# Kernel tuning notes

Measured on AMD Instinct MI355X. Metric: run time of the kernel, lower is better.

The kernel has to match this reference:

```python
import jax, jax.numpy as jnp
import numpy as np
from jax import lax

T, B, D, H = 1024, 64, 512, 512


def _elman_layer(x_seq, Wih, bih, Whh, bhh):
    """x_seq: [T, B, in]; returns hidden sequence [T, B, out].
    Input-side GEMM is precomputed across all timesteps; the recurrence
    (h @ Whh^T + bhh, tanh) runs in a lax.scan with state resident.
    """
    xs = jnp.einsum('tbi,hi->tbh', x_seq, Wih) + bih  # [T, B, H]
    h0 = jnp.zeros((x_seq.shape[1], Whh.shape[0]), dtype=x_seq.dtype)

    def step(h, xt):
        h_new = jnp.tanh(xt + h @ Whh.T + bhh)
        return h_new, h_new

    _, ys = lax.scan(step, h0, xs)
    return ys


def setup_inputs() -> dict:
    key = jax.random.key(0)
    ks = jax.random.split(key, 9)
    stdv = 1.0 / np.sqrt(H)
    u = lambda k, shape: jax.random.uniform(k, shape, jnp.float32, -stdv, stdv)
    return {
        'Xt': jax.random.normal(ks[0], (T, B, D), jnp.float32),
        'ihW0': u(ks[1], (H, D)),
        'ihB0': u(ks[2], (H,)),
        'hhW0': u(ks[3], (H, H)),
        'hhB0': u(ks[4], (H,)),
        'ihW1': u(ks[5], (H, H)),
        'ihB1': u(ks[6], (H,)),
        'hhW1': u(ks[7], (H, H)),
        'hhB1': u(ks[8], (H,)),
    }


def reference(Xt, ihW0, ihB0, hhW0, hhB0, ihW1, ihB1, hhW1, hhB1):
    # 2-layer Elman RNN, tanh activation, zero initial hidden state,
    # dropout=0 (eval), stack_output=True -> output [T, B, H].
    y0 = _elman_layer(Xt, ihW0, ihB0, hhW0, hhB0)
    y1 = _elman_layer(y0, ihW1, ihB1, hhW1, hhB1)
    return y1
```

## Files before the change

kernel.cpp:

```cpp
#include <hip/hip_runtime.h>
#include <math.h>
#include <stdint.h>

#define TT      1024
#define BATCH   64
#define HH      512
#define NG      8
#define WPG     32
#define BSL     8
#define HSL     16
#define NTH     512

#define WBLK(m, jj, u)  ((((m) * 2 + (jj)) * 4 + (u)) << 10)
#define WLDS    (24 * 1024)
#define SPW     516
#define BUFH0   WLDS
#define BUFH1   (WLDS + 8 * SPW)
#define SCR     (WLDS + 16 * SPW)
#define SCRS    17
#define LDS_FL  (SCR + 129 * SCRS)
#define LDS_BYTES (LDS_FL * 4)

__device__ __forceinline__ float2 sys_ld2(const float* p) {
    unsigned long long v = __hip_atomic_load((const unsigned long long*)p, __ATOMIC_RELAXED,
                                             __HIP_MEMORY_SCOPE_SYSTEM);
    union { unsigned long long u; float2 f; } cv; cv.u = v; return cv.f;
}
__device__ __forceinline__ void sys_st(float* p, float v) {
    __hip_atomic_store(p, v, __ATOMIC_RELAXED, __HIP_MEMORY_SCOPE_SYSTEM);
}
__device__ __forceinline__ void wait_vm0() {
    asm volatile("s_waitcnt vmcnt(0)" ::: "memory");
}
__device__ __forceinline__ void dot4(float4 w, float4 x, float& a) {
    a = fmaf(w.x, x.x, a); a = fmaf(w.y, x.y, a);
    a = fmaf(w.z, x.z, a); a = fmaf(w.w, x.w, a);
}

__global__ void __launch_bounds__(256)
z0_gemm(const float* __restrict__ X, const float* __restrict__ W,
        const float* __restrict__ bih, float* __restrict__ Z)
{
    __shared__ float As[32][68];
    __shared__ float Bs[32][68];
    const int tid = threadIdx.x;
    const int tx  = tid & 15, ty = tid >> 4;
    const int n0  = (blockIdx.x & 7) * 64;
    const int m0  = (blockIdx.x >> 3) * 64;
    const int lm  = tid >> 3;
    const int lk  = (tid & 7) * 4;

    float4 bb;
    bb.x = bih[n0 + tx * 4 + 0]; bb.y = bih[n0 + tx * 4 + 1];
    bb.z = bih[n0 + tx * 4 + 2]; bb.w = bih[n0 + tx * 4 + 3];

    float acc[4][4];
    #pragma unroll
    for (int i = 0; i < 4; ++i)
        #pragma unroll
        for (int j = 0; j < 4; ++j) acc[i][j] = 0.f;

    for (int k0 = 0; k0 < 512; k0 += 32) {
        float4 a0 = *(const float4*)(X + (size_t)(m0 + lm) * 512 + k0 + lk);
        float4 a1 = *(const float4*)(X + (size_t)(m0 + lm + 32) * 512 + k0 + lk);
        float4 b0 = *(const float4*)(W + (size_t)(n0 + lm) * 512 + k0 + lk);
        float4 b1 = *(const float4*)(W + (size_t)(n0 + lm + 32) * 512 + k0 + lk);
        __syncthreads();
        As[lk + 0][lm] = a0.x; As[lk + 1][lm] = a0.y;
        As[lk + 2][lm] = a0.z; As[lk + 3][lm] = a0.w;
        As[lk + 0][lm + 32] = a1.x; As[lk + 1][lm + 32] = a1.y;
        As[lk + 2][lm + 32] = a1.z; As[lk + 3][lm + 32] = a1.w;
        Bs[lk + 0][lm] = b0.x; Bs[lk + 1][lm] = b0.y;
        Bs[lk + 2][lm] = b0.z; Bs[lk + 3][lm] = b0.w;
        Bs[lk + 0][lm + 32] = b1.x; Bs[lk + 1][lm + 32] = b1.y;
        Bs[lk + 2][lm + 32] = b1.z; Bs[lk + 3][lm + 32] = b1.w;
        __syncthreads();
        #pragma unroll
        for (int kk = 0; kk < 32; ++kk) {
            float4 av = *(const float4*)(&As[kk][ty * 4]);
            float4 bv = *(const float4*)(&Bs[kk][tx * 4]);
            acc[0][0] = fmaf(av.x, bv.x, acc[0][0]); acc[0][1] = fmaf(av.x, bv.y, acc[0][1]);
            acc[0][2] = fmaf(av.x, bv.z, acc[0][2]); acc[0][3] = fmaf(av.x, bv.w, acc[0][3]);
            acc[1][0] = fmaf(av.y, bv.x, acc[1][0]); acc[1][1] = fmaf(av.y, bv.y, acc[1][1]);
            acc[1][2] = fmaf(av.y, bv.z, acc[1][2]); acc[1][3] = fmaf(av.y, bv.w, acc[1][3]);
            acc[2][0] = fmaf(av.z, bv.x, acc[2][0]); acc[2][1] = fmaf(av.z, bv.y, acc[2][1]);
            acc[2][2] = fmaf(av.z, bv.z, acc[2][2]); acc[2][3] = fmaf(av.z, bv.w, acc[2][3]);
            acc[3][0] = fmaf(av.w, bv.x, acc[3][0]); acc[3][1] = fmaf(av.w, bv.y, acc[3][1]);
            acc[3][2] = fmaf(av.w, bv.z, acc[3][2]); acc[3][3] = fmaf(av.w, bv.w, acc[3][3]);
        }
    }
    #pragma unroll
    for (int i = 0; i < 4; ++i) {
        float4 r;
        r.x = acc[i][0] + bb.x; r.y = acc[i][1] + bb.y;
        r.z = acc[i][2] + bb.z; r.w = acc[i][3] + bb.w;
        *(float4*)(Z + (size_t)(m0 + ty * 4 + i) * 512 + n0 + tx * 4) = r;
    }
}

__global__ void __launch_bounds__(NTH, 2)
elman_persistent(const float* __restrict__ Whh0, const float* __restrict__ bhh0,
                 const float* __restrict__ Wih1, const float* __restrict__ bih1,
                 const float* __restrict__ Whh1, const float* __restrict__ bhh1,
                 float* __restrict__ out,
                 float* h0buf,
                 unsigned* cnt)
{
    extern __shared__ float lds[];
    const int tid = threadIdx.x;
    const int g   = blockIdx.x & 7;
    const int w   = blockIdx.x >> 3;
    const int jg0 = w * HSL;
    const int bg0 = g * BSL;

    const int jp   = tid & 7;
    const int bb4  = ((tid >> 3) & 1) * 4;
    const int ks   = tid >> 4;
    const int kb   = ks * 4;
    const int wofs = ks * 32 + jp * 4;
    const int lane = tid & 63;
    const int wv   = tid >> 6;

    const int row = tid >> 6;
    const int kst = (tid & 63) * 4;

    {
        const float* const Ws[3] = {Whh0, Wih1, Whh1};
        for (int f = tid; f < 48 * 128; f += NTH) {
            const int jrow = f >> 7, k4 = f & 127;
            const int mat = jrow >> 4, r = jrow & 15;
            const int jp_ = r >> 1, jj_ = r & 1;
            const int u_ = k4 >> 5, ks_ = k4 & 31;
            float4 v = ((const float4*)(Ws[mat] + (size_t)(jg0 + r) * HH))[k4];
            *(float4*)(lds + WBLK(mat, jj_, u_) + ks_ * 32 + jp_ * 4) = v;
        }
    }
    float bias = 0.f;
    if (tid < 256) {
        const int l = tid >> 7, jx = jg0 + (tid & 15);
        bias = l ? (bih1[jx] + bhh1[jx]) : bhh0[jx];
    }
    __syncthreads();

    const float* h1load = out + (size_t)(bg0 + row) * HH + kst;

    unsigned* mycnt = cnt + g * 64;
    unsigned target = 0;
    bool     dead   = false;

    for (int p = 0; p <= TT; ++p) {
        const bool doL0  = (p < TT);
        const bool doL1  = (p >= 1);
        const bool hasH1 = (p >= 2);
        const int  cur   = p & 1;

        float2 h0a, h0b, h0c, h0d;
        {
            const float* hs = h0buf + (size_t)((p + 1) & 1) * (BATCH * HH)
                            + (size_t)(bg0 + row) * HH + kst;
            h0a = sys_ld2(hs);       h0b = sys_ld2(hs + 2);
            h0c = sys_ld2(hs + 256); h0d = sys_ld2(hs + 258);
        }
        float2 h1a = {0.f, 0.f}, h1b = h1a, h1c = h1a, h1d = h1a;
        if (hasH1) {
            h1a = sys_ld2(h1load);       h1b = sys_ld2(h1load + 2);
            h1c = sys_ld2(h1load + 256); h1d = sys_ld2(h1load + 258);
            h1load += BATCH * HH;
        }
        float z0v = 0.f;
        if (doL0 && tid < 128)
            z0v = out[((size_t)p * BATCH + bg0 + (tid >> 4)) * HH + jg0 + (tid & 15)];

        wait_vm0();
        *(float4*)(lds + BUFH0 + row * SPW + kst)       = make_float4(h0a.x, h0a.y, h0b.x, h0b.y);
        *(float4*)(lds + BUFH0 + row * SPW + kst + 256) = make_float4(h0c.x, h0c.y, h0d.x, h0d.y);
        if (hasH1) {
            *(float4*)(lds + BUFH1 + row * SPW + kst)       = make_float4(h1a.x, h1a.y, h1b.x, h1b.y);
            *(float4*)(lds + BUFH1 + row * SPW + kst + 256) = make_float4(h1c.x, h1c.y, h1d.x, h1d.y);
        }
        __syncthreads();

        float acc0[2][4], acc1[2][4];
        #pragma unroll
        for (int jj = 0; jj < 2; ++jj)
            #pragma unroll
            for (int bi = 0; bi < 4; ++bi) { acc0[jj][bi] = 0.f; acc1[jj][bi] = 0.f; }

        auto h0pass = [&](bool d0, bool d1) {
            #pragma unroll
            for (int u = 0; u < 4; ++u) {
                float4 wa0 = *(const float4*)(lds + WBLK(0, 0, u) + wofs);
                float4 wa1 = *(const float4*)(lds + WBLK(0, 1, u) + wofs);
                float4 wb0 = *(const float4*)(lds + WBLK(1, 0, u) + wofs);
                float4 wb1 = *(const float4*)(lds + WBLK(1, 1, u) + wofs);
                #pragma unroll
                for (int bi = 0; bi < 4; ++bi) {
                    float4 hv = *(const float4*)(lds + BUFH0 + (bb4 + bi) * SPW + kb + u * 128);
                    if (d0) { dot4(wa0, hv, acc0[0][bi]);
                              dot4(wa1, hv, acc0[1][bi]); }
                    if (d1) { dot4(wb0, hv, acc1[0][bi]);
                              dot4(wb1, hv, acc1[1][bi]); }
                }
            }
        };
        if (doL0 && doL1) h0pass(true, true);
        else if (doL0)    h0pass(true, false);
        else              h0pass(false, true);
        if (hasH1) {
            #pragma unroll
            for (int u = 0; u < 4; ++u) {
                float4 wc0 = *(const float4*)(lds + WBLK(2, 0, u) + wofs);
                float4 wc1 = *(const float4*)(lds + WBLK(2, 1, u) + wofs);
                #pragma unroll
                for (int bi = 0; bi < 4; ++bi) {
                    float4 hv = *(const float4*)(lds + BUFH1 + (bb4 + bi) * SPW + kb + u * 128);
                    dot4(wc0, hv, acc1[0][bi]);
                    dot4(wc1, hv, acc1[1][bi]);
                }
            }
        }

        #pragma unroll
        for (int jj = 0; jj < 2; ++jj)
            #pragma unroll
            for (int bi = 0; bi < 4; ++bi) {
                acc0[jj][bi] += __shfl_xor(acc0[jj][bi], 16);
                acc0[jj][bi] += __shfl_xor(acc0[jj][bi], 32);
                acc1[jj][bi] += __shfl_xor(acc1[jj][bi], 16);
                acc1[jj][bi] += __shfl_xor(acc1[jj][bi], 32);
            }
        if (lane < 16) {
            #pragma unroll
            for (int jj = 0; jj < 2; ++jj)
                #pragma unroll
                for (int bi = 0; bi < 4; ++bi) {
                    lds[SCR + (wv * 16 + jj * 4 + bi) * SCRS + lane]     = acc0[jj][bi];
                    lds[SCR + (wv * 16 + 8 + jj * 4 + bi) * SCRS + lane] = acc1[jj][bi];
                }
        }
        __syncthreads();

        if (tid < 256) {
            const int l    = tid >> 7;
            const int jloc = tid & 15;
            const int blo  = (tid >> 4) & 7;
            const int a    = l * 8 + (jloc & 1) * 4 + (blo & 3);
            const int ll   = (jloc >> 1) + 8 * (blo >> 2);
            float s = 0.f;
            #pragma unroll
            for (int wq = 0; wq < 8; ++wq)
                s += lds[SCR + (wq * 16 + a) * SCRS + ll];
            float val = tanhf(s + bias + z0v);
            if (l == 0) {
                if (doL0) sys_st(h0buf + (size_t)cur * (BATCH * HH)
                                 + (size_t)(bg0 + blo) * HH + jg0 + jloc, val);
            } else {
                if (doL1) sys_st(out + ((size_t)(p - 1) * BATCH + bg0 + blo) * HH + jg0 + jloc, val);
            }
        }
        wait_vm0();
        __syncthreads();

        if (tid == 0) {
            __hip_atomic_fetch_add(mycnt, 1u, __ATOMIC_RELAXED, __HIP_MEMORY_SCOPE_SYSTEM);
            target += WPG;
            if (!dead) {
                unsigned spins = 0;
                while (__hip_atomic_load(mycnt, __ATOMIC_RELAXED, __HIP_MEMORY_SCOPE_SYSTEM) < target) {
                    __builtin_amdgcn_s_sleep(2);
                    if (++spins > (1u << 21)) { dead = true; break; }
                }
            }
            asm volatile("" ::: "memory");
        } else {
            target += WPG;
        }
        __syncthreads();
    }
}

extern "C" void kernel_launch(void* const* d_in, const int* in_sizes, int n_in,
                              void* d_out, int out_size, void* d_ws, size_t ws_size,
                              hipStream_t stream) {
    (void)in_sizes; (void)n_in; (void)out_size; (void)ws_size;
    const float* Xt   = (const float*)d_in[0];
    const float* Wih0 = (const float*)d_in[1];
    const float* bih0 = (const float*)d_in[2];
    const float* Whh0 = (const float*)d_in[3];
    const float* bhh0 = (const float*)d_in[4];
    const float* Wih1 = (const float*)d_in[5];
    const float* bih1 = (const float*)d_in[6];
    const float* Whh1 = (const float*)d_in[7];
    const float* bhh1 = (const float*)d_in[8];
    float*    out   = (float*)d_out;
    float*    h0buf = (float*)d_ws;
    unsigned* cnt   = (unsigned*)((char*)d_ws + 2 * BATCH * HH * 4);

    hipFuncSetAttribute((const void*)elman_persistent,
                        hipFuncAttributeMaxDynamicSharedMemorySize, LDS_BYTES);
    hipMemsetAsync(d_ws, 0, 2 * BATCH * HH * 4 + NG * 256, stream);

    z0_gemm<<<dim3((TT * BATCH / 64) * (HH / 64)), dim3(256), 0, stream>>>(
        Xt, Wih0, bih0, out);

    elman_persistent<<<dim3(NG * WPG), dim3(NTH), LDS_BYTES, stream>>>(
        Whh0, bhh0, Wih1, bih1, Whh1, bhh1, out, h0buf, cnt);
}
```

Before: 6.995 ms.

## Load hidden states directly into registers, skip LDS staging and prefetch input projection

Each thread now loads the exact h0 and h1 slices it needs from global memory straight into registers, rather than staging full rows into LDS and reading them back. This drops the LDS staging buffers and one __syncthreads per step. The precomputed input term for the next step is also prefetched one step early to hide its latency. The cost is more redundant global loads, since threads sharing batch rows each fetch them, and higher register pressure from 32 float4 values. The h0 pass now always computes both layers' products, even on the boundary steps, where that work was previously skipped.

```diff
diff --git a/kernel.cpp b/kernel.cpp
--- a/kernel.cpp
+++ b/kernel.cpp
@@ -13,10 +13,7 @@
 
 #define WBLK(m, jj, u)  ((((m) * 2 + (jj)) * 4 + (u)) << 10)
 #define WLDS    (24 * 1024)
-#define SPW     516
-#define BUFH0   WLDS
-#define BUFH1   (WLDS + 8 * SPW)
-#define SCR     (WLDS + 16 * SPW)
+#define SCR     WLDS
 #define SCRS    17
 #define LDS_FL  (SCR + 129 * SCRS)
 #define LDS_BYTES (LDS_FL * 4)
@@ -121,9 +118,6 @@
     const int lane = tid & 63;
     const int wv   = tid >> 6;
 
-    const int row = tid >> 6;
-    const int kst = (tid & 63) * 4;
-
     {
         const float* const Ws[3] = {Whh0, Wih1, Whh1};
         for (int f = tid; f < 48 * 128; f += NTH) {
@@ -140,9 +134,10 @@
         const int l = tid >> 7, jx = jg0 + (tid & 15);
         bias = l ? (bih1[jx] + bhh1[jx]) : bhh0[jx];
     }
+    float z0cur = 0.f;
+    if (tid < 128)
+        z0cur = out[(size_t)(bg0 + (tid >> 4)) * HH + jg0 + (tid & 15)];
     __syncthreads();
-
-    const float* h1load = out + (size_t)(bg0 + row) * HH + kst;
 
     unsigned* mycnt = cnt + g * 64;
     unsigned target = 0;
@@ -154,31 +149,38 @@
         const bool hasH1 = (p >= 2);
         const int  cur   = p & 1;
 
-        float2 h0a, h0b, h0c, h0d;
+        float4 h0r[4][4];
         {
-            const float* hs = h0buf + (size_t)((p + 1) & 1) * (BATCH * HH)
-                            + (size_t)(bg0 + row) * HH + kst;
-            h0a = sys_ld2(hs);       h0b = sys_ld2(hs + 2);
-            h0c = sys_ld2(hs + 256); h0d = sys_ld2(hs + 258);
-        }
-        float2 h1a = {0.f, 0.f}, h1b = h1a, h1c = h1a, h1d = h1a;
+            const float* b0 = h0buf + (size_t)((p + 1) & 1) * (BATCH * HH)
+                            + (size_t)(bg0 + bb4) * HH + kb;
+            #pragma unroll
+            for (int bi = 0; bi < 4; ++bi) {
+                const float* pp = b0 + bi * HH;
+                #pragma unroll
+                for (int u = 0; u < 4; ++u) {
+                    float2 lo = sys_ld2(pp + u * 128);
+                    float2 hi = sys_ld2(pp + u * 128 + 2);
+                    h0r[bi][u] = make_float4(lo.x, lo.y, hi.x, hi.y);
+                }
+            }
+        }
+        float4 h1r[4][4];
         if (hasH1) {
-            h1a = sys_ld2(h1load);       h1b = sys_ld2(h1load + 2);
-            h1c = sys_ld2(h1load + 256); h1d = sys_ld2(h1load + 258);
-            h1load += BATCH * HH;
-        }
-        float z0v = 0.f;
-        if (doL0 && tid < 128)
-            z0v = out[((size_t)p * BATCH + bg0 + (tid >> 4)) * HH + jg0 + (tid & 15)];
-
-        wait_vm0();
-        *(float4*)(lds + BUFH0 + row * SPW + kst)       = make_float4(h0a.x, h0a.y, h0b.x, h0b.y);
-        *(float4*)(lds + BUFH0 + row * SPW + kst + 256) = make_float4(h0c.x, h0c.y, h0d.x, h0d.y);
-        if (hasH1) {
-            *(float4*)(lds + BUFH1 + row * SPW + kst)       = make_float4(h1a.x, h1a.y, h1b.x, h1b.y);
-            *(float4*)(lds + BUFH1 + row * SPW + kst + 256) = make_float4(h1c.x, h1c.y, h1d.x, h1d.y);
-        }
-        __syncthreads();
+            const float* b1 = out + ((size_t)(p - 2) * BATCH + bg0 + bb4) * HH + kb;
+            #pragma unroll
+            for (int bi = 0; bi < 4; ++bi) {
+                const float* pp = b1 + bi * HH;
+                #pragma unroll
+                for (int u = 0; u < 4; ++u) {
+                    float2 lo = sys_ld2(pp + u * 128);
+                    float2 hi = sys_ld2(pp + u * 128 + 2);
+                    h1r[bi][u] = make_float4(lo.x, lo.y, hi.x, hi.y);
+                }
+            }
+        }
+        float z0n = 0.f;
+        if (p + 1 < TT && tid < 128)
+            z0n = out[((size_t)(p + 1) * BATCH + bg0 + (tid >> 4)) * HH + jg0 + (tid & 15)];
 
         float acc0[2][4], acc1[2][4];
         #pragma unroll
@@ -186,26 +188,21 @@
             #pragma unroll
             for (int bi = 0; bi < 4; ++bi) { acc0[jj][bi] = 0.f; acc1[jj][bi] = 0.f; }
 
-        auto h0pass = [&](bool d0, bool d1) {
-            #pragma unroll
-            for (int u = 0; u < 4; ++u) {
-                float4 wa0 = *(const float4*)(lds + WBLK(0, 0, u) + wofs);
-                float4 wa1 = *(const float4*)(lds + WBLK(0, 1, u) + wofs);
-                float4 wb0 = *(const float4*)(lds + WBLK(1, 0, u) + wofs);
-                float4 wb1 = *(const float4*)(lds + WBLK(1, 1, u) + wofs);
-                #pragma unroll
-                for (int bi = 0; bi < 4; ++bi) {
-                    float4 hv = *(const float4*)(lds + BUFH0 + (bb4 + bi) * SPW + kb + u * 128);
-                    if (d0) { dot4(wa0, hv, acc0[0][bi]);
-                              dot4(wa1, hv, acc0[1][bi]); }
-                    if (d1) { dot4(wb0, hv, acc1[0][bi]);
-                              dot4(wb1, hv, acc1[1][bi]); }
-                }
-            }
-        };
-        if (doL0 && doL1) h0pass(true, true);
-        else if (doL0)    h0pass(true, false);
-        else              h0pass(false, true);
+        #pragma unroll
+        for (int u = 0; u < 4; ++u) {
+            float4 wa0 = *(const float4*)(lds + WBLK(0, 0, u) + wofs);
+            float4 wa1 = *(const float4*)(lds + WBLK(0, 1, u) + wofs);
+            float4 wb0 = *(const float4*)(lds + WBLK(1, 0, u) + wofs);
+            float4 wb1 = *(const float4*)(lds + WBLK(1, 1, u) + wofs);
+            #pragma unroll
+            for (int bi = 0; bi < 4; ++bi) {
+                float4 hv = h0r[bi][u];
+                dot4(wa0, hv, acc0[0][bi]);
+                dot4(wa1, hv, acc0[1][bi]);
+                dot4(wb0, hv, acc1[0][bi]);
+                dot4(wb1, hv, acc1[1][bi]);
+            }
+        }
         if (hasH1) {
             #pragma unroll
             for (int u = 0; u < 4; ++u) {
@@ -213,7 +210,7 @@
                 float4 wc1 = *(const float4*)(lds + WBLK(2, 1, u) + wofs);
                 #pragma unroll
                 for (int bi = 0; bi < 4; ++bi) {
-                    float4 hv = *(const float4*)(lds + BUFH1 + (bb4 + bi) * SPW + kb + u * 128);
+                    float4 hv = h1r[bi][u];
                     dot4(wc0, hv, acc1[0][bi]);
                     dot4(wc1, hv, acc1[1][bi]);
                 }
@@ -250,7 +247,7 @@
             #pragma unroll
             for (int wq = 0; wq < 8; ++wq)
                 s += lds[SCR + (wq * 16 + a) * SCRS + ll];
-            float val = tanhf(s + bias + z0v);
+            float val = tanhf(s + bias + (l ? 0.f : z0cur));
             if (l == 0) {
                 if (doL0) sys_st(h0buf + (size_t)cur * (BATCH * HH)
                                  + (size_t)(bg0 + blo) * HH + jg0 + jloc, val);
@@ -258,6 +255,7 @@
                 if (doL1) sys_st(out + ((size_t)(p - 1) * BATCH + bg0 + blo) * HH + jg0 + jloc, val);
             }
         }
+        z0cur = z0n;
         wait_vm0();
         __syncthreads();
 
```

After: 7.818 ms. 1.12x slower.
